# Kernel tuning notes

Measured on AMD Instinct MI355X. Metric: run time of the kernel, lower is better.

The kernel has to match this reference:

```python
import jax, jax.numpy as jnp
import numpy as np

CLASS_NUM = 2      # init_kwargs class_num
NUM_WEIGHTS = 3    # distinct values present in weighted_target (torch.unique)
SHAPE = (16, 2048, 2048)


def setup_inputs() -> dict:
    key = jax.random.key(0)
    k1, k2, k3 = jax.random.split(key, 3)
    pred = jax.random.uniform(k1, SHAPE, dtype=jnp.float32)
    target = jax.random.randint(k2, SHAPE, 0, CLASS_NUM).astype(jnp.int32)
    weighted_target = jax.random.randint(k3, SHAPE, 0, NUM_WEIGHTS).astype(jnp.int32)
    return {"pred": pred, "target": target, "weighted_target": weighted_target}


def reference(pred, target, weighted_target):
    # Original double loop over (class i, unique weight j):
    #   mask = (target==i) & (weighted_target==j); n = sum(mask)
    #   numerator   += sum(pred[mask]) / n^2
    #   denominator += sum((pred + mask)[mask]) / n^2 = (sum(pred[mask]) + n) / n^2
    # loss = 1 - 2*numerator/denominator
    # Single-pass segmented reduction over bucket id = class*W + weight.
    W = NUM_WEIGHTS
    nseg = CLASS_NUM * W
    seg = (target * W + weighted_target).reshape(-1)   # [N] bucket ids
    p = pred.reshape(-1)                               # [N]
    counts = jax.ops.segment_sum(jnp.ones_like(p), seg, num_segments=nseg)  # [nseg]
    psum = jax.ops.segment_sum(p, seg, num_segments=nseg)                   # [nseg]
    inv_n2 = jnp.where(counts > 0, 1.0 / (counts * counts), 0.0)
    numerator = jnp.sum(psum * inv_n2)
    denominator = jnp.sum((psum + counts) * inv_n2)
    return 1.0 - 2.0 * numerator / denominator
```

## Files before the change

kernel.cpp:

```cpp
#include <hip/hip_runtime.h>

#define NSEG 6
#define NBLOCKS 2048
#define NTHREADS 256

__global__ __launch_bounds__(NTHREADS) void wdice_partial(
    const float4* __restrict__ pred,
    const int4* __restrict__ tgt,
    const int4* __restrict__ wt,
    int nvec,
    float* __restrict__ psum_out,
    float* __restrict__ cnt_out)
{
    float ps[NSEG];
    float cn[NSEG];
#pragma unroll
    for (int s = 0; s < NSEG; ++s) { ps[s] = 0.f; cn[s] = 0.f; }

    int tid = blockIdx.x * blockDim.x + threadIdx.x;
    int stride = gridDim.x * blockDim.x;
    for (int i = tid; i < nvec; i += stride) {
        float4 p = pred[i];
        int4 t = tgt[i];
        int4 w = wt[i];
        int seg0 = t.x * 3 + w.x;
        int seg1 = t.y * 3 + w.y;
        int seg2 = t.z * 3 + w.z;
        int seg3 = t.w * 3 + w.w;
#pragma unroll
        for (int s = 0; s < NSEG; ++s) {
            if (seg0 == s) { ps[s] += p.x; cn[s] += 1.f; }
            if (seg1 == s) { ps[s] += p.y; cn[s] += 1.f; }
            if (seg2 == s) { ps[s] += p.z; cn[s] += 1.f; }
            if (seg3 == s) { ps[s] += p.w; cn[s] += 1.f; }
        }
    }

#pragma unroll
    for (int s = 0; s < NSEG; ++s) {
#pragma unroll
        for (int off = 32; off > 0; off >>= 1) {
            ps[s] += __shfl_down(ps[s], off, 64);
            cn[s] += __shfl_down(cn[s], off, 64);
        }
    }

    __shared__ float lps[4][NSEG];
    __shared__ float lcn[4][NSEG];
    int lane = threadIdx.x & 63;
    int wave = threadIdx.x >> 6;
    if (lane == 0) {
#pragma unroll
        for (int s = 0; s < NSEG; ++s) { lps[wave][s] = ps[s]; lcn[wave][s] = cn[s]; }
    }
    __syncthreads();
    if (threadIdx.x == 0) {
#pragma unroll
        for (int s = 0; s < NSEG; ++s) {
            float tps = lps[0][s] + lps[1][s] + lps[2][s] + lps[3][s];
            float tcn = lcn[0][s] + lcn[1][s] + lcn[2][s] + lcn[3][s];
            psum_out[blockIdx.x * NSEG + s] = tps;
            cnt_out[blockIdx.x * NSEG + s] = tcn;
        }
    }
}

__global__ __launch_bounds__(NTHREADS) void wdice_final(
    const float* __restrict__ psum_in,
    const float* __restrict__ cnt_in,
    int nrows,
    float* __restrict__ out)
{
    double ps[NSEG];
    double cn[NSEG];
#pragma unroll
    for (int s = 0; s < NSEG; ++s) { ps[s] = 0.0; cn[s] = 0.0; }

    for (int r = threadIdx.x; r < nrows; r += blockDim.x) {
#pragma unroll
        for (int s = 0; s < NSEG; ++s) {
            ps[s] += (double)psum_in[r * NSEG + s];
            cn[s] += (double)cnt_in[r * NSEG + s];
        }
    }

#pragma unroll
    for (int s = 0; s < NSEG; ++s) {
#pragma unroll
        for (int off = 32; off > 0; off >>= 1) {
            ps[s] += __shfl_down(ps[s], off, 64);
            cn[s] += __shfl_down(cn[s], off, 64);
        }
    }

    __shared__ double lps[4][NSEG];
    __shared__ double lcn[4][NSEG];
    int lane = threadIdx.x & 63;
    int wave = threadIdx.x >> 6;
    if (lane == 0) {
#pragma unroll
        for (int s = 0; s < NSEG; ++s) { lps[wave][s] = ps[s]; lcn[wave][s] = cn[s]; }
    }
    __syncthreads();
    if (threadIdx.x == 0) {
        double numer = 0.0, denom = 0.0;
#pragma unroll
        for (int s = 0; s < NSEG; ++s) {
            double tps = lps[0][s] + lps[1][s] + lps[2][s] + lps[3][s];
            double tcn = lcn[0][s] + lcn[1][s] + lcn[2][s] + lcn[3][s];
            if (tcn > 0.0) {
                double inv_n2 = 1.0 / (tcn * tcn);
                numer += tps * inv_n2;
                denom += (tps + tcn) * inv_n2;
            }
        }
        out[0] = (float)(1.0 - 2.0 * numer / denom);
    }
}

extern "C" void kernel_launch(void* const* d_in, const int* in_sizes, int n_in,
                              void* d_out, int out_size, void* d_ws, size_t ws_size,
                              hipStream_t stream) {
    const float4* pred = (const float4*)d_in[0];
    const int4* tgt = (const int4*)d_in[1];
    const int4* wt = (const int4*)d_in[2];
    int n = in_sizes[0];
    int nvec = n / 4;

    float* psum_ws = (float*)d_ws;
    float* cnt_ws = psum_ws + NBLOCKS * NSEG;

    wdice_partial<<<NBLOCKS, NTHREADS, 0, stream>>>(pred, tgt, wt, nvec, psum_ws, cnt_ws);
    wdice_final<<<1, NTHREADS, 0, stream>>>(psum_ws, cnt_ws, NBLOCKS, (float*)d_out);
}
```

Before: 151.0 us.

## Unroll loads 4x and count segments with packed 8-bit integer counters

Result: no change. 152.5 us (+1.0%).

```diff
diff --git a/kernel.cpp b/kernel.cpp
--- a/kernel.cpp
+++ b/kernel.cpp
@@ -4,110 +4,160 @@
 #define NBLOCKS 2048
 #define NTHREADS 256
 
+__device__ __forceinline__ void proc4(const float4& p, const int4& t, const int4& w,
+                                      float ps[NSEG], unsigned long long& c64) {
+    int s0 = t.x * 3 + w.x;
+    int s1 = t.y * 3 + w.y;
+    int s2 = t.z * 3 + w.z;
+    int s3 = t.w * 3 + w.w;
+    c64 += (1ull << (s0 << 3)) + (1ull << (s1 << 3)) +
+           (1ull << (s2 << 3)) + (1ull << (s3 << 3));
+#pragma unroll
+    for (int s = 0; s < NSEG; ++s) {
+        float v = (s0 == s ? p.x : 0.f);
+        v += (s1 == s ? p.y : 0.f);
+        v += (s2 == s ? p.z : 0.f);
+        v += (s3 == s ? p.w : 0.f);
+        ps[s] += v;
+    }
+}
+
 __global__ __launch_bounds__(NTHREADS) void wdice_partial(
     const float4* __restrict__ pred,
     const int4* __restrict__ tgt,
     const int4* __restrict__ wt,
     int nvec,
-    float* __restrict__ psum_out,
-    float* __restrict__ cnt_out)
+    float* __restrict__ out_ws)
 {
     float ps[NSEG];
-    float cn[NSEG];
+    int cn[NSEG];
 #pragma unroll
-    for (int s = 0; s < NSEG; ++s) { ps[s] = 0.f; cn[s] = 0.f; }
+    for (int s = 0; s < NSEG; ++s) { ps[s] = 0.f; cn[s] = 0; }
 
-    int tid = blockIdx.x * blockDim.x + threadIdx.x;
-    int stride = gridDim.x * blockDim.x;
-    for (int i = tid; i < nvec; i += stride) {
+    const int tid = threadIdx.x;
+    const int stride = NBLOCKS * NTHREADS;
+    int i = blockIdx.x * NTHREADS + tid;
+
+    while (i + 3 * stride < nvec) {
+        unsigned long long c64 = 0ull;
+        for (int chunk = 0; chunk < 15 && i + 3 * stride < nvec; ++chunk, i += 4 * stride) {
+            float4 p0 = pred[i];
+            float4 p1 = pred[i + stride];
+            float4 p2 = pred[i + 2 * stride];
+            float4 p3 = pred[i + 3 * stride];
+            int4 t0 = tgt[i];
+            int4 t1 = tgt[i + stride];
+            int4 t2 = tgt[i + 2 * stride];
+            int4 t3 = tgt[i + 3 * stride];
+            int4 w0 = wt[i];
+            int4 w1 = wt[i + stride];
+            int4 w2 = wt[i + 2 * stride];
+            int4 w3 = wt[i + 3 * stride];
+
+            proc4(p0, t0, w0, ps, c64);
+            proc4(p1, t1, w1, ps, c64);
+            proc4(p2, t2, w2, ps, c64);
+            proc4(p3, t3, w3, ps, c64);
+        }
+#pragma unroll
+        for (int s = 0; s < NSEG; ++s) cn[s] += (int)((c64 >> (8 * s)) & 0xFFull);
+    }
+    for (; i < nvec; i += stride) {
         float4 p = pred[i];
         int4 t = tgt[i];
         int4 w = wt[i];
-        int seg0 = t.x * 3 + w.x;
-        int seg1 = t.y * 3 + w.y;
-        int seg2 = t.z * 3 + w.z;
-        int seg3 = t.w * 3 + w.w;
+        int s0 = t.x * 3 + w.x;
+        int s1 = t.y * 3 + w.y;
+        int s2 = t.z * 3 + w.z;
+        int s3 = t.w * 3 + w.w;
 #pragma unroll
         for (int s = 0; s < NSEG; ++s) {
-            if (seg0 == s) { ps[s] += p.x; cn[s] += 1.f; }
-            if (seg1 == s) { ps[s] += p.y; cn[s] += 1.f; }
-            if (seg2 == s) { ps[s] += p.z; cn[s] += 1.f; }
-            if (seg3 == s) { ps[s] += p.w; cn[s] += 1.f; }
+            cn[s] += (s0 == s) + (s1 == s) + (s2 == s) + (s3 == s);
+            float v = (s0 == s ? p.x : 0.f);
+            v += (s1 == s ? p.y : 0.f);
+            v += (s2 == s ? p.z : 0.f);
+            v += (s3 == s ? p.w : 0.f);
+            ps[s] += v;
         }
     }
 
+    unsigned int pk0 = (unsigned)cn[0] | ((unsigned)cn[1] << 16);
+    unsigned int pk1 = (unsigned)cn[2] | ((unsigned)cn[3] << 16);
+    unsigned int pk2 = (unsigned)cn[4] | ((unsigned)cn[5] << 16);
+
 #pragma unroll
-    for (int s = 0; s < NSEG; ++s) {
+    for (int off = 32; off > 0; off >>= 1) {
 #pragma unroll
-        for (int off = 32; off > 0; off >>= 1) {
-            ps[s] += __shfl_down(ps[s], off, 64);
-            cn[s] += __shfl_down(cn[s], off, 64);
-        }
+        for (int s = 0; s < NSEG; ++s) ps[s] += __shfl_down(ps[s], off, 64);
+        pk0 += __shfl_down(pk0, off, 64);
+        pk1 += __shfl_down(pk1, off, 64);
+        pk2 += __shfl_down(pk2, off, 64);
     }
 
     __shared__ float lps[4][NSEG];
-    __shared__ float lcn[4][NSEG];
+    __shared__ unsigned int lpk[4][3];
+    int lane = tid & 63;
+    int wave = tid >> 6;
+    if (lane == 0) {
+#pragma unroll
+        for (int s = 0; s < NSEG; ++s) lps[wave][s] = ps[s];
+        lpk[wave][0] = pk0; lpk[wave][1] = pk1; lpk[wave][2] = pk2;
+    }
+    __syncthreads();
+    if (tid == 0) {
+        unsigned int bk0 = lpk[0][0] + lpk[1][0] + lpk[2][0] + lpk[3][0];
+        unsigned int bk1 = lpk[0][1] + lpk[1][1] + lpk[2][1] + lpk[3][1];
+        unsigned int bk2 = lpk[0][2] + lpk[1][2] + lpk[2][2] + lpk[3][2];
+#pragma unroll
+        for (int s = 0; s < NSEG; ++s) {
+            float tps = lps[0][s] + lps[1][s] + lps[2][s] + lps[3][s];
+            out_ws[blockIdx.x * 12 + s] = tps;
+        }
+        out_ws[blockIdx.x * 12 + 6]  = (float)(bk0 & 0xFFFF);
+        out_ws[blockIdx.x * 12 + 7]  = (float)(bk0 >> 16);
+        out_ws[blockIdx.x * 12 + 8]  = (float)(bk1 & 0xFFFF);
+        out_ws[blockIdx.x * 12 + 9]  = (float)(bk1 >> 16);
+        out_ws[blockIdx.x * 12 + 10] = (float)(bk2 & 0xFFFF);
+        out_ws[blockIdx.x * 12 + 11] = (float)(bk2 >> 16);
+    }
+}
+
+__global__ __launch_bounds__(NTHREADS) void wdice_final(
+    const float* __restrict__ ws,
+    int nrows,
+    float* __restrict__ out)
+{
+    double a[12];
+#pragma unroll
+    for (int r = 0; r < 12; ++r) a[r] = 0.0;
+
+    for (int row = threadIdx.x; row < nrows; row += blockDim.x) {
+#pragma unroll
+        for (int r = 0; r < 12; ++r)
+            a[r] += (double)ws[row * 12 + r];
+    }
+
+#pragma unroll
+    for (int r = 0; r < 12; ++r) {
+#pragma unroll
+        for (int off = 32; off > 0; off >>= 1)
+            a[r] += __shfl_down(a[r], off, 64);
+    }
+
+    __shared__ double l[4][12];
     int lane = threadIdx.x & 63;
     int wave = threadIdx.x >> 6;
     if (lane == 0) {
 #pragma unroll
-        for (int s = 0; s < NSEG; ++s) { lps[wave][s] = ps[s]; lcn[wave][s] = cn[s]; }
-    }
-    __syncthreads();
-    if (threadIdx.x == 0) {
-#pragma unroll
-        for (int s = 0; s < NSEG; ++s) {
-            float tps = lps[0][s] + lps[1][s] + lps[2][s] + lps[3][s];
-            float tcn = lcn[0][s] + lcn[1][s] + lcn[2][s] + lcn[3][s];
-            psum_out[blockIdx.x * NSEG + s] = tps;
-            cnt_out[blockIdx.x * NSEG + s] = tcn;
-        }
-    }
-}
-
-__global__ __launch_bounds__(NTHREADS) void wdice_final(
-    const float* __restrict__ psum_in,
-    const float* __restrict__ cnt_in,
-    int nrows,
-    float* __restrict__ out)
-{
-    double ps[NSEG];
-    double cn[NSEG];
-#pragma unroll
-    for (int s = 0; s < NSEG; ++s) { ps[s] = 0.0; cn[s] = 0.0; }
-
-    for (int r = threadIdx.x; r < nrows; r += blockDim.x) {
-#pragma unroll
-        for (int s = 0; s < NSEG; ++s) {
-            ps[s] += (double)psum_in[r * NSEG + s];
-            cn[s] += (double)cnt_in[r * NSEG + s];
-        }
-    }
-
-#pragma unroll
-    for (int s = 0; s < NSEG; ++s) {
-#pragma unroll
-        for (int off = 32; off > 0; off >>= 1) {
-            ps[s] += __shfl_down(ps[s], off, 64);
-            cn[s] += __shfl_down(cn[s], off, 64);
-        }
-    }
-
-    __shared__ double lps[4][NSEG];
-    __shared__ double lcn[4][NSEG];
-    int lane = threadIdx.x & 63;
-    int wave = threadIdx.x >> 6;
-    if (lane == 0) {
-#pragma unroll
-        for (int s = 0; s < NSEG; ++s) { lps[wave][s] = ps[s]; lcn[wave][s] = cn[s]; }
+        for (int r = 0; r < 12; ++r) l[wave][r] = a[r];
     }
     __syncthreads();
     if (threadIdx.x == 0) {
         double numer = 0.0, denom = 0.0;
 #pragma unroll
         for (int s = 0; s < NSEG; ++s) {
-            double tps = lps[0][s] + lps[1][s] + lps[2][s] + lps[3][s];
-            double tcn = lcn[0][s] + lcn[1][s] + lcn[2][s] + lcn[3][s];
+            double tps = l[0][s] + l[1][s] + l[2][s] + l[3][s];
+            double tcn = l[0][s + 6] + l[1][s + 6] + l[2][s + 6] + l[3][s + 6];
             if (tcn > 0.0) {
                 double inv_n2 = 1.0 / (tcn * tcn);
                 numer += tps * inv_n2;
@@ -127,9 +177,8 @@
     int n = in_sizes[0];
     int nvec = n / 4;
 
-    float* psum_ws = (float*)d_ws;
-    float* cnt_ws = psum_ws + NBLOCKS * NSEG;
+    float* ws = (float*)d_ws;
 
-    wdice_partial<<<NBLOCKS, NTHREADS, 0, stream>>>(pred, tgt, wt, nvec, psum_ws, cnt_ws);
-    wdice_final<<<1, NTHREADS, 0, stream>>>(psum_ws, cnt_ws, NBLOCKS, (float*)d_out);
+    wdice_partial<<<NBLOCKS, NTHREADS, 0, stream>>>(pred, tgt, wt, nvec, ws);
+    wdice_final<<<1, NTHREADS, 0, stream>>>(ws, NBLOCKS, (float*)d_out);
 }
```
